# Kernel tuning notes

Measured on AMD Instinct MI355X. Metric: run time of the kernel, lower is better.

Reference implementation:

```python
import jax, jax.numpy as jnp
import numpy as np

N_PP, BATCH, BITS = 54, 16384, 108  # 54 partial products of a 54x54 array multiplier, 108-bit lanes


def setup_inputs() -> dict:
    key = jax.random.key(0)
    # bits are {0,1} floats, LSB-first along the last axis
    pps = jax.random.randint(key, (N_PP, BATCH, BITS), 0, 2).astype(jnp.float32)
    return {"pps": pps}


def _ripple_add(a, b):
    """Bit-exact ripple-carry add over last (bits) axis, LSB first.

    a, b: [..., BITS] with values in {0,1}. Returns (sum [..., BITS], carry_out [...]).
    Boolean full adder expressed arithmetically so it is differentiable:
      xor(x,y) = x + y - 2xy ; and(x,y) = xy ; or(x,y) = x + y - xy
    """
    aT = jnp.moveaxis(a, -1, 0)  # [BITS, ...]
    bT = jnp.moveaxis(b, -1, 0)
    c0 = jnp.zeros(a.shape[:-1], a.dtype)

    def full_adder(c, ab):
        ai, bi = ab
        axb = ai + bi - 2.0 * ai * bi          # a XOR b
        s = axb + c - 2.0 * axb * c            # (a XOR b) XOR c
        g = ai * bi                            # generate
        p = axb * c                            # propagate AND carry
        c_next = g + p - g * p                 # g OR p
        return c_next, s

    c_out, sT = jax.lax.scan(full_adder, c0, (aT, bT))
    return jnp.moveaxis(sT, 0, -1), c_out


def reference(pps):
    """Sequential (mode='sequential') accumulation of partial products.

    pps: [N_PP, ..., BITS]. result = (((pp0 + pp1) + pp2) + ...), bit-exact,
    carry-out dropped at each step exactly as in the torch module.
    """
    def step(res, p):
        s, _ = _ripple_add(res, p)
        return s, None

    out, _ = jax.lax.scan(step, pps[0], pps[1:])
    return out
```

## Files before the change

### kernel.cpp

```cpp
#include <hip/hip_runtime.h>


#define N_PP   54
#define BITS   108
#define BATCH  16384
#define ROW_F4 (BITS / 4)
#define PLANE_F4 ((size_t)BATCH * ROW_F4)

typedef float vf4 __attribute__((ext_vector_type(4)));

__global__ __launch_bounds__(256)
void count_kernel(const vf4* __restrict__ pps, vf4* __restrict__ cnt) {
    const size_t i0 = (size_t)blockIdx.x * 256 + threadIdx.x;
    const vf4* p = pps + i0;

    vf4 acc = (vf4)(0.f);

    vf4 v0 = __builtin_nontemporal_load(p + 0 * PLANE_F4);
    vf4 v1 = __builtin_nontemporal_load(p + 1 * PLANE_F4);
    vf4 v2 = __builtin_nontemporal_load(p + 2 * PLANE_F4);
    vf4 v3 = __builtin_nontemporal_load(p + 3 * PLANE_F4);

    for (int q = 4; q + 4 <= N_PP - 2; q += 4) {
        const vf4* pq = p + (size_t)q * PLANE_F4;
        vf4 n0 = __builtin_nontemporal_load(pq + 0 * PLANE_F4);
        vf4 n1 = __builtin_nontemporal_load(pq + 1 * PLANE_F4);
        vf4 n2 = __builtin_nontemporal_load(pq + 2 * PLANE_F4);
        vf4 n3 = __builtin_nontemporal_load(pq + 3 * PLANE_F4);
        acc += v0; acc += v1; acc += v2; acc += v3;
        v0 = n0; v1 = n1; v2 = n2; v3 = n3;
    }

    vf4 e0 = __builtin_nontemporal_load(p + (size_t)(N_PP - 2) * PLANE_F4);
    vf4 e1 = __builtin_nontemporal_load(p + (size_t)(N_PP - 1) * PLANE_F4);
    acc += v0; acc += v1; acc += v2; acc += v3;
    acc += e0; acc += e1;

    cnt[i0] = acc;
}

__global__ __launch_bounds__(64)
void carry_kernel(vf4* __restrict__ buf) {
    const int row = blockIdx.x * 64 + threadIdx.x;
    vf4* rp = buf + (size_t)row * ROW_F4;

    float r[BITS];
#pragma unroll
    for (int j = 0; j < ROW_F4; ++j) {
        reinterpret_cast<vf4*>(r)[j] = rp[j];
    }

    int c = 0;
#pragma unroll
    for (int i = 0; i < BITS; ++i) {
        const int t = (int)r[i] + c;
        r[i] = (float)(t & 1);
        c = t >> 1;
    }

#pragma unroll
    for (int j = 0; j < ROW_F4; ++j) {
        rp[j] = reinterpret_cast<vf4*>(r)[j];
    }
}

extern "C" void kernel_launch(void* const* d_in, const int* in_sizes, int n_in,
                              void* d_out, int out_size, void* d_ws, size_t ws_size,
                              hipStream_t stream) {
    const vf4* pps = (const vf4*)d_in[0];
    vf4* out = (vf4*)d_out;

    count_kernel<<<(int)(PLANE_F4 / 256), 256, 0, stream>>>(pps, out);
    carry_kernel<<<BATCH / 64, 64, 0, stream>>>(out);
}
```

Baseline: 469.2 us.

## Fuse column counting and carry propagation into one kernel via shared memory

Merges the count kernel and the carry kernel into one launch. Each block of 432 threads covers 16 full rows, stages the per-bit column counts in LDS, resolves carries serially with 16 threads, then writes the final bits back. This drops the second launch and the global round trip of the count buffer. In exchange, the carry ripple runs on only 16 threads per block while the rest wait at a barrier, and the block size is not a multiple of 64.

```diff
diff --git a/kernel.cpp b/kernel.cpp
--- a/kernel.cpp
+++ b/kernel.cpp
@@ -6,12 +6,17 @@
 #define BATCH  16384
 #define ROW_F4 (BITS / 4)
 #define PLANE_F4 ((size_t)BATCH * ROW_F4)
+#define ROWS_PB 16
+#define TPB     (ROWS_PB * ROW_F4)
 
 typedef float vf4 __attribute__((ext_vector_type(4)));
 
-__global__ __launch_bounds__(256)
-void count_kernel(const vf4* __restrict__ pps, vf4* __restrict__ cnt) {
-    const size_t i0 = (size_t)blockIdx.x * 256 + threadIdx.x;
+__global__ __launch_bounds__(TPB)
+void ppacc_fused(const vf4* __restrict__ pps, vf4* __restrict__ out) {
+    __shared__ float counts[ROWS_PB][BITS + 1];
+
+    const int tid = threadIdx.x;
+    const size_t i0 = (size_t)blockIdx.x * TPB + tid;
     const vf4* p = pps + i0;
 
     vf4 acc = (vf4)(0.f);
@@ -30,37 +35,41 @@
         acc += v0; acc += v1; acc += v2; acc += v3;
         v0 = n0; v1 = n1; v2 = n2; v3 = n3;
     }
-
     vf4 e0 = __builtin_nontemporal_load(p + (size_t)(N_PP - 2) * PLANE_F4);
     vf4 e1 = __builtin_nontemporal_load(p + (size_t)(N_PP - 1) * PLANE_F4);
     acc += v0; acc += v1; acc += v2; acc += v3;
     acc += e0; acc += e1;
 
-    cnt[i0] = acc;
-}
+    {
+        const int row = tid / ROW_F4;
+        const int bit = (tid % ROW_F4) * 4;
+        counts[row][bit + 0] = acc.x;
+        counts[row][bit + 1] = acc.y;
+        counts[row][bit + 2] = acc.z;
+        counts[row][bit + 3] = acc.w;
+    }
+    __syncthreads();
 
-__global__ __launch_bounds__(64)
-void carry_kernel(vf4* __restrict__ buf) {
-    const int row = blockIdx.x * 64 + threadIdx.x;
-    vf4* rp = buf + (size_t)row * ROW_F4;
+    if (tid < ROWS_PB) {
+        int c = 0;
+#pragma unroll
+        for (int i = 0; i < BITS; ++i) {
+            const int t = (int)counts[tid][i] + c;
+            counts[tid][i] = (float)(t & 1);
+            c = t >> 1;
+        }
+    }
+    __syncthreads();
 
-    float r[BITS];
-#pragma unroll
-    for (int j = 0; j < ROW_F4; ++j) {
-        reinterpret_cast<vf4*>(r)[j] = rp[j];
-    }
-
-    int c = 0;
-#pragma unroll
-    for (int i = 0; i < BITS; ++i) {
-        const int t = (int)r[i] + c;
-        r[i] = (float)(t & 1);
-        c = t >> 1;
-    }
-
-#pragma unroll
-    for (int j = 0; j < ROW_F4; ++j) {
-        rp[j] = reinterpret_cast<vf4*>(r)[j];
+    {
+        const int row = tid / ROW_F4;
+        const int bit = (tid % ROW_F4) * 4;
+        vf4 v;
+        v.x = counts[row][bit + 0];
+        v.y = counts[row][bit + 1];
+        v.z = counts[row][bit + 2];
+        v.w = counts[row][bit + 3];
+        out[i0] = v;
     }
 }
 
@@ -69,7 +78,5 @@
                               hipStream_t stream) {
     const vf4* pps = (const vf4*)d_in[0];
     vf4* out = (vf4*)d_out;
-
-    count_kernel<<<(int)(PLANE_F4 / 256), 256, 0, stream>>>(pps, out);
-    carry_kernel<<<BATCH / 64, 64, 0, stream>>>(out);
+    ppacc_fused<<<(int)(PLANE_F4 / TPB), TPB, 0, stream>>>(pps, out);
 }
```

Measured after the change: 462.3 us, median of 2. No clear change (-1.5%).
